# Performance work log

Measured on AMD Instinct MI355X. Metric: run time of the kernel, lower is better.

The kernel has to match this reference:

```python
import jax, jax.numpy as jnp
import numpy as np

N = 20000      # nodes
E = 200000     # edges (before self loops)
H = 8          # heads
C = 256        # out_channels per head
IN = 256       # in_channels
OUT = 250      # final linear out


def setup_inputs() -> dict:
    key = jax.random.key(0)
    ks = jax.random.split(key, 8)
    x = jax.random.normal(ks[0], (N, IN), jnp.float32)
    edge_index = jax.random.randint(ks[1], (2, E), 0, N)
    # GATConv params (lin has no bias in PyG; bias is on the conv output)
    W_gat = jax.random.normal(ks[2], (IN, H * C), jnp.float32) * 0.02
    att_src = jax.random.normal(ks[3], (H, C), jnp.float32) * 0.1
    att_dst = jax.random.normal(ks[4], (H, C), jnp.float32) * 0.1
    b_gat = jnp.zeros((H * C,), jnp.float32)
    # conv1: 1x1 conv with 1 in/out channel -> scalar weight + scalar bias
    conv_w = jax.random.normal(ks[5], (), jnp.float32)
    conv_b = jnp.zeros((), jnp.float32)
    W_lin = jax.random.normal(ks[6], (C, OUT), jnp.float32) * 0.02
    b_lin = jnp.zeros((OUT,), jnp.float32)
    return dict(x=x, edge_index=edge_index, W_gat=W_gat, att_src=att_src,
                att_dst=att_dst, b_gat=b_gat, conv_w=conv_w, conv_b=conv_b,
                W_lin=W_lin, b_lin=b_lin)


def reference(x, edge_index, W_gat, att_src, att_dst, b_gat, conv_w, conv_b, W_lin, b_lin):
    # --- GATConv (PyG defaults: add_self_loops=True, negative_slope=0.2, concat=True) ---
    loops = jnp.arange(N)
    src = jnp.concatenate([edge_index[0], loops])  # [E+N]
    dst = jnp.concatenate([edge_index[1], loops])
    xh = (x @ W_gat).reshape(N, H, C)              # [N,H,C]
    a_s = jnp.einsum('nhc,hc->nh', xh, att_src)    # [N,H]
    a_d = jnp.einsum('nhc,hc->nh', xh, att_dst)
    e = jax.nn.leaky_relu(a_s[src] + a_d[dst], 0.2)  # [E+N, H]
    # segment softmax over edges sharing a destination node
    m = jax.ops.segment_max(e, dst, num_segments=N)
    m = jnp.where(jnp.isfinite(m), m, 0.0)
    ex = jnp.exp(e - m[dst])
    s = jax.ops.segment_sum(ex, dst, num_segments=N)
    alpha = ex / (s[dst] + 1e-16)                  # [E+N, H]
    msg = xh[src] * alpha[:, :, None]              # [E+N, H, C]  (dominant traffic)
    agg = jax.ops.segment_sum(msg, dst, num_segments=N)  # [N,H,C]
    agg = agg + b_gat.reshape(H, C)
    # --- head split / pool / 1x1 conv / head softmax / fuse ---
    z = agg.transpose(1, 0, 2)                     # [H,N,C]  (torch z is [H,1,N,C])
    pooled = z.mean(axis=(1, 2))                   # [H] global avg pool
    g = jax.nn.relu(pooled * conv_w + conv_b)
    w = jax.nn.softmax(g, axis=0)                  # softmax over heads (dim=0)
    fuse = jnp.einsum('hnc,h->nc', z, w)           # sum over heads of z * w
    Hf = jax.nn.relu(fuse + x)                     # residual with input features
    return Hf @ W_lin + b_lin                      # [N, 250]
```

## Files before the change

### kernel.cpp

```cpp
#include <hip/hip_runtime.h>
#include <hip/hip_bf16.h>


typedef __attribute__((ext_vector_type(8))) short short8v;
typedef __attribute__((ext_vector_type(4))) float float4v;

__device__ __forceinline__ unsigned f2bfu(float f) {
  unsigned u = __float_as_uint(f);
  return (u + 0x7fffu + ((u >> 16) & 1u)) >> 16;
}
__device__ __forceinline__ float bfu_lo(unsigned u) { return __uint_as_float(u << 16); }
__device__ __forceinline__ float bfu_hi(unsigned u) { return __uint_as_float(u & 0xffff0000u); }
__device__ __forceinline__ unsigned pack2(float a, float b) { return f2bfu(a) | (f2bfu(b) << 16); }

__device__ __forceinline__ void ld8(const float* p, float* v) {
  float4 a = ((const float4*)p)[0], b = ((const float4*)p)[1];
  v[0] = a.x; v[1] = a.y; v[2] = a.z; v[3] = a.w;
  v[4] = b.x; v[5] = b.y; v[6] = b.z; v[7] = b.w;
}

__device__ __forceinline__ float bcast(float x, int e) {
  return __uint_as_float((unsigned)__builtin_amdgcn_readlane((int)__float_as_uint(x), e));
}

__device__ __forceinline__ void gll16(const void* g, void* l) {
  __builtin_amdgcn_global_load_lds(
      (__attribute__((address_space(1))) void*)const_cast<void*>(g),
      (__attribute__((address_space(3))) void*)(l), 16, 0, 0);
}

__global__ __launch_bounds__(256) void prep1_kernel(
    const float* __restrict__ W_lin, short* __restrict__ wlT,
    const float* __restrict__ W, const float* __restrict__ att_s,
    const float* __restrict__ att_d, float* __restrict__ ws_s,
    float* __restrict__ ws_d, float* __restrict__ ws_r,
    const int* __restrict__ ei, int* __restrict__ deg) {
  __shared__ float smem[4096];
  int b = blockIdx.x;
  int t = threadIdx.x;
  if (b < 64) {
    float (*tile)[33] = (float(*)[33])smem;
    int tx = t & 31, ty = t >> 5;
    int c0 = (b & 7) * 32, r0 = (b >> 3) * 32;
    #pragma unroll
    for (int j = ty; j < 32; j += 8) {
      int r = r0 + j, c = c0 + tx;
      tile[j][tx] = (c < 250) ? W_lin[(size_t)r * 250 + c] : 0.f;
    }
    __syncthreads();
    #pragma unroll
    for (int j = ty; j < 32; j += 8) {
      int c = c0 + j, r = r0 + tx;
      wlT[(size_t)c * 256 + r] = (short)f2bfu(tile[tx][j]);
    }
  } else if (b < 96) {
    float* sas = smem;
    float* sad = smem + 2048;
    for (int i = t; i < 2048; i += 256) { sas[i] = att_s[i]; sad[i] = att_d[i]; }
    __syncthreads();
    int kk = t >> 5, h = (t >> 2) & 7, q = t & 3;
    int k = (b - 64) * 8 + kk;
    const float4* wr = (const float4*)(W + (size_t)k * 2048 + h * 256 + q * 64);
    const float* as = sas + h * 256 + q * 64;
    const float* ad = sad + h * 256 + q * 64;
    float s = 0.f, dd = 0.f, r = 0.f;
    #pragma unroll
    for (int c4 = 0; c4 < 16; ++c4) {
      float4 wv = wr[c4];
      int c = c4 * 4;
      s  += wv.x * as[c] + wv.y * as[c + 1] + wv.z * as[c + 2] + wv.w * as[c + 3];
      dd += wv.x * ad[c] + wv.y * ad[c + 1] + wv.z * ad[c + 2] + wv.w * ad[c + 3];
      r  += wv.x + wv.y + wv.z + wv.w;
    }
    #pragma unroll
    for (int off = 1; off < 4; off <<= 1) {
      s += __shfl_xor(s, off);
      dd += __shfl_xor(dd, off);
      r += __shfl_xor(r, off);
    }
    if (q == 0) {
      int g = k * 8 + h;
      ws_s[g] = s;
      ws_d[g] = dd;
      ws_r[g] = r;
    }
  } else {
    int e = (b - 96) * 256 + t;
    if (e < 200000) atomicAdd(&deg[ei[200000 + e]], 1);
  }
}

__global__ __launch_bounds__(256) void asd_kernel(const float* __restrict__ x,
    const float* __restrict__ ws_s, const float* __restrict__ ws_d,
    float* __restrict__ a_s, float* __restrict__ a_d, short* __restrict__ x_bf) {
  __shared__ float ls[2048], ld2[2048];
  int tid = threadIdx.x;
  for (int i = tid; i < 2048; i += 256) { ls[i] = ws_s[i]; ld2[i] = ws_d[i]; }
  __syncthreads();
  int node = blockIdx.x * 32 + (tid >> 3);
  int h = tid & 7;
  const float4* xr = (const float4*)(x + (size_t)node * 256);
  float as = 0.f, ad = 0.f;
  #pragma unroll 1
  for (int g = 0; g < 8; ++g) {
    bool own = (g == h);
    int bufi[16];
    #pragma unroll
    for (int j = 0; j < 8; ++j) {
      int k4 = g * 8 + j;
      float4 v = xr[k4];
      int k8 = k4 * 32 + h;
      as += v.x * ls[k8] + v.y * ls[k8 + 8] + v.z * ls[k8 + 16] + v.w * ls[k8 + 24];
      ad += v.x * ld2[k8] + v.y * ld2[k8 + 8] + v.z * ld2[k8 + 16] + v.w * ld2[k8 + 24];
      bufi[2 * j] = (int)pack2(v.x, v.y);
      bufi[2 * j + 1] = (int)pack2(v.z, v.w);
    }
    if (own) {
      int4* dst = (int4*)(x_bf + (size_t)node * 256 + h * 32);
      dst[0] = make_int4(bufi[0], bufi[1], bufi[2], bufi[3]);
      dst[1] = make_int4(bufi[4], bufi[5], bufi[6], bufi[7]);
      dst[2] = make_int4(bufi[8], bufi[9], bufi[10], bufi[11]);
      dst[3] = make_int4(bufi[12], bufi[13], bufi[14], bufi[15]);
    }
  }
  a_s[node * 8 + h] = as;
  a_d[node * 8 + h] = ad;
}

template <int EPI>
__global__ __launch_bounds__(256, 4) void gemm_kernel(
    const short* __restrict__ A, const short* __restrict__ BT,
    int M, int K,
    short* __restrict__ Cb, float* __restrict__ Cf,
    const float* __restrict__ bias, const float* __restrict__ xres, int Nout) {
  int g = blockIdx.x;
  int xk = g & 7, tt = g >> 3;
  int it = xk + 8 * (tt >> 2);
  if (it >= ((M + 63) >> 6)) return;
  int m0 = it << 6;
  int n0 = (tt & 3) << 6;

  __shared__ short lA[64 * 64];
  __shared__ short lB[64 * 64];
  int tid = threadIdx.x;
  int wave = tid >> 6, lane = tid & 63;
  int wm = wave >> 1, wn = wave & 1;
  int lr = lane & 15, lq = lane >> 4;

  float4v acc[2][2];
  #pragma unroll
  for (int i = 0; i < 2; ++i)
    #pragma unroll
    for (int j = 0; j < 2; ++j) acc[i][j] = (float4v){0.f, 0.f, 0.f, 0.f};

  int lc = (lane & 7) ^ (lane >> 3);
  const short* pA[2];
  const short* pB[2];
  #pragma unroll
  for (int p = 0; p < 2; ++p) {
    int rl = wave * 16 + p * 8 + (lane >> 3);
    int ar = m0 + rl;
    if (ar >= M) ar = M - 1;
    pA[p] = A + (size_t)ar * K + lc * 8;
    pB[p] = BT + (size_t)(n0 + rl) * K + lc * 8;
  }

  for (int k0 = 0; k0 < K; k0 += 64) {
    __syncthreads();
    #pragma unroll
    for (int p = 0; p < 2; ++p) {
      gll16(pA[p] + k0, lA + (wave * 16 + p * 8) * 64);
      gll16(pB[p] + k0, lB + (wave * 16 + p * 8) * 64);
    }
    __syncthreads();
    #pragma unroll
    for (int ks = 0; ks < 2; ++ks) {
      int phys = (((ks * 4 + lq) ^ (lr & 7))) * 8;
      short8v af[2], bfv[2];
      #pragma unroll
      for (int i = 0; i < 2; ++i)
        af[i] = *(const short8v*)(lA + (wm * 32 + i * 16 + lr) * 64 + phys);
      #pragma unroll
      for (int j = 0; j < 2; ++j)
        bfv[j] = *(const short8v*)(lB + (wn * 32 + j * 16 + lr) * 64 + phys);
      #pragma unroll
      for (int i = 0; i < 2; ++i)
        #pragma unroll
        for (int j = 0; j < 2; ++j)
          acc[i][j] = __builtin_amdgcn_mfma_f32_16x16x32_bf16(af[i], bfv[j], acc[i][j], 0, 0, 0);
    }
  }

  #pragma unroll
  for (int i = 0; i < 2; ++i) {
    #pragma unroll
    for (int jj = 0; jj < 4; ++jj) {
      int row = m0 + wm * 32 + i * 16 + lq * 4 + jj;
      if (row >= M) continue;
      #pragma unroll
      for (int j = 0; j < 2; ++j) {
        int col = n0 + wn * 32 + j * 16 + lr;
        float v = acc[i][j][jj];
        if (EPI == 1) {
          if (col < Nout) Cf[(size_t)row * Nout + col] = v + bias[col];
        } else {
          float o = v + bias[col] + xres[(size_t)row * 256 + col];
          Cb[(size_t)row * 256 + col] = (short)f2bfu(fmaxf(o, 0.f));
        }
      }
    }
  }
}


__global__ __launch_bounds__(1024) void scan_kernel(const int* __restrict__ deg,
                                                    int* __restrict__ rowptr,
                                                    int* __restrict__ cursor, int n) {
  __shared__ int part[1024];
  int t = threadIdx.x;
  int base = t * 20;
  int loc[20];
  int run = 0;
  #pragma unroll
  for (int j = 0; j < 20; ++j) {
    int idx = base + j;
    int v = (idx < n) ? deg[idx] : 0;
    loc[j] = run;
    run += v;
  }
  part[t] = run;
  __syncthreads();
  for (int off = 1; off < 1024; off <<= 1) {
    int add = (t >= off) ? part[t - off] : 0;
    __syncthreads();
    part[t] += add;
    __syncthreads();
  }
  int off0 = (t > 0) ? part[t - 1] : 0;
  #pragma unroll
  for (int j = 0; j < 20; ++j) {
    int idx = base + j;
    if (idx < n) {
      int v = off0 + loc[j];
      rowptr[idx] = v;
      cursor[idx] = v;
    }
  }
  if (t == 1023) rowptr[n] = part[1023];
}

__global__ void scatter_kernel(const int* __restrict__ ei, int* __restrict__ cursor,
                               int* __restrict__ csr_src, int E) {
  int e = blockIdx.x * 256 + threadIdx.x;
  if (e < E) {
    int pos = atomicAdd(&cursor[ei[E + e]], 1);
    csr_src[pos] = ei[e];
  }
}

__global__ __launch_bounds__(64) void alphaz_kernel(
    const short* __restrict__ x_bf, const float* __restrict__ a_s,
    const float* __restrict__ a_d, const float* __restrict__ ws_r,
    const int* __restrict__ rowptr, const int* __restrict__ csr,
    short* __restrict__ u, float* __restrict__ pp) {
  int d = blockIdx.x;
  int lane = threadIdx.x;
  int cl = lane * 4;
  int beg = rowptr[d];
  int deg = rowptr[d + 1] - beg;
  int nb = deg + 1;

  float ad8[8];
  ld8(a_d + (size_t)d * 8, ad8);

  float acc[8][4];
  #pragma unroll
  for (int h = 0; h < 8; ++h)
    #pragma unroll
    for (int c = 0; c < 4; ++c) acc[h][c] = 0.f;
  float s8[8] = {0, 0, 0, 0, 0, 0, 0, 0};

  for (int base = 0; base < nb; base += 64) {
    int i = base + lane;
    bool act = i < nb;
    int srcv = d;
    if (i < deg) srcv = csr[beg + i];
    float ex[8];
    {
      float t8[8];
      ld8(a_s + (size_t)srcv * 8, t8);
      #pragma unroll
      for (int h = 0; h < 8; ++h) {
        float e = t8[h] + ad8[h];
        e = (e > 0.f) ? e : 0.2f * e;
        float xx = act ? __expf(e) : 0.f;
        ex[h] = xx;
        s8[h] += xx;
      }
    }
    int cnt = nb - base;
    if (cnt > 64) cnt = 64;
    for (int e = 0; e < cnt; ++e) {
      int sb = __builtin_amdgcn_readlane(srcv, e);
      uint2 v = *(const uint2*)(x_bf + (size_t)sb * 256 + cl);
      float q[8];
      #pragma unroll
      for (int h = 0; h < 8; ++h) q[h] = bcast(ex[h], e);
      float xv0 = bfu_lo(v.x), xv1 = bfu_hi(v.x);
      float xv2 = bfu_lo(v.y), xv3 = bfu_hi(v.y);
      #pragma unroll
      for (int h = 0; h < 8; ++h) {
        acc[h][0] += q[h] * xv0;
        acc[h][1] += q[h] * xv1;
        acc[h][2] += q[h] * xv2;
        acc[h][3] += q[h] * xv3;
      }
    }
  }

  #pragma unroll
  for (int off = 1; off < 64; off <<= 1)
    #pragma unroll
    for (int h = 0; h < 8; ++h) s8[h] += __shfl_xor(s8[h], off);
  float inv[8];
  #pragma unroll
  for (int h = 0; h < 8; ++h) inv[h] = 1.f / (s8[h] + 1e-16f);

  #pragma unroll
  for (int h = 0; h < 8; ++h) {
    uint2 ov;
    ov.x = pack2(acc[h][0] * inv[h], acc[h][1] * inv[h]);
    ov.y = pack2(acc[h][2] * inv[h], acc[h][3] * inv[h]);
    *(uint2*)(u + (size_t)d * 2048 + h * 256 + cl) = ov;
  }

  float ppl[8] = {0, 0, 0, 0, 0, 0, 0, 0};
  {
    const float4* wr = (const float4*)(ws_r + (size_t)cl * 8);
    #pragma unroll
    for (int c = 0; c < 4; ++c) {
      float4 wa = wr[c * 2], wb = wr[c * 2 + 1];
      float zc[8];
      #pragma unroll
      for (int h = 0; h < 8; ++h) zc[h] = acc[h][c] * inv[h];
      ppl[0] += zc[0] * wa.x; ppl[1] += zc[1] * wa.y;
      ppl[2] += zc[2] * wa.z; ppl[3] += zc[3] * wa.w;
      ppl[4] += zc[4] * wb.x; ppl[5] += zc[5] * wb.y;
      ppl[6] += zc[6] * wb.z; ppl[7] += zc[7] * wb.w;
    }
  }
  #pragma unroll
  for (int off = 1; off < 64; off <<= 1)
    #pragma unroll
    for (int h = 0; h < 8; ++h) ppl[h] += __shfl_xor(ppl[h], off);
  if (lane == 0) {
    ((float4*)(pp + (size_t)d * 8))[0] = make_float4(ppl[0], ppl[1], ppl[2], ppl[3]);
    ((float4*)(pp + (size_t)d * 8))[1] = make_float4(ppl[4], ppl[5], ppl[6], ppl[7]);
  }
}

__global__ __launch_bounds__(256) void reduce_pp_kernel(const float* __restrict__ pp,
                                                        float* __restrict__ pooled) {
  int tid = threadIdx.x;
  float loc[8] = {0, 0, 0, 0, 0, 0, 0, 0};
  for (int r = blockIdx.x * 256 + tid; r < 20000; r += 80 * 256) {
    float t[8];
    ld8(pp + (size_t)r * 8, t);
    #pragma unroll
    for (int h = 0; h < 8; ++h) loc[h] += t[h];
  }
  #pragma unroll
  for (int off = 1; off < 64; off <<= 1)
    #pragma unroll
    for (int h = 0; h < 8; ++h) loc[h] += __shfl_xor(loc[h], off);
  __shared__ float sred[4][8];
  int wave = tid >> 6, lane = tid & 63;
  if (lane == 0) {
    #pragma unroll
    for (int h = 0; h < 8; ++h) sred[wave][h] = loc[h];
  }
  __syncthreads();
  if (tid < 8) {
    atomicAdd(&pooled[tid], sred[0][tid] + sred[1][tid] + sred[2][tid] + sred[3][tid]);
  }
}

__global__ __launch_bounds__(256) void headwfb_kernel(const float* __restrict__ pooled,
    const float* __restrict__ b_gat, const float* __restrict__ conv_w,
    const float* __restrict__ conv_b, float* __restrict__ wsoft,
    float* __restrict__ fb) {
  __shared__ float sb[8];
  __shared__ float sw[8];
  int t = threadIdx.x;
  float v = 0.f;
  #pragma unroll
  for (int j = 0; j < 8; ++j) v += b_gat[t * 8 + j];
  #pragma unroll
  for (int off = 1; off < 32; off <<= 1) v += __shfl_xor(v, off);
  if ((t & 31) == 0) sb[t >> 5] = v;
  __syncthreads();
  if (t == 0) {
    const float invNC = 1.0f / (20000.0f * 256.0f);
    float g[8];
    float mx = -1e30f;
    #pragma unroll
    for (int h = 0; h < 8; ++h) {
      float pm = (pooled[h] + 20000.0f * sb[h]) * invNC;
      float gv = pm * conv_w[0] + conv_b[0];
      gv = fmaxf(gv, 0.f);
      g[h] = gv;
      mx = fmaxf(mx, gv);
    }
    float ssum = 0.f;
    #pragma unroll
    for (int h = 0; h < 8; ++h) { g[h] = __expf(g[h] - mx); ssum += g[h]; }
    #pragma unroll
    for (int h = 0; h < 8; ++h) {
      float w = g[h] / ssum;
      wsoft[h] = w;
      sw[h] = w;
    }
  }
  __syncthreads();
  float a = 0.f;
  #pragma unroll
  for (int h = 0; h < 8; ++h) a += sw[h] * b_gat[h * 256 + t];
  fb[t] = a;
}

__global__ void wmix_kernel(const float* __restrict__ W, const float* __restrict__ wsoft,
                            short* __restrict__ out) {
  __shared__ float tile[32][33];
  int tx = threadIdx.x, ty = threadIdx.y;
  int h = blockIdx.z;
  float wh = wsoft[h];
  int c0 = blockIdx.x * 32, k0 = blockIdx.y * 32;
  #pragma unroll
  for (int j = ty; j < 32; j += 8)
    tile[j][tx] = W[(size_t)(k0 + j) * 2048 + h * 256 + c0 + tx];
  __syncthreads();
  #pragma unroll
  for (int j = ty; j < 32; j += 8)
    out[(size_t)(c0 + j) * 2048 + h * 256 + k0 + tx] = (short)f2bfu(wh * tile[tx][j]);
}

extern "C" void kernel_launch(void* const* d_in, const int* in_sizes, int n_in,
                              void* d_out, int out_size, void* d_ws, size_t ws_size,
                              hipStream_t stream) {
  (void)in_sizes; (void)n_in; (void)out_size; (void)ws_size;
  const float* x      = (const float*)d_in[0];
  const int*   ei     = (const int*)d_in[1];
  const float* W_gat  = (const float*)d_in[2];
  const float* att_s  = (const float*)d_in[3];
  const float* att_d  = (const float*)d_in[4];
  const float* b_gat  = (const float*)d_in[5];
  const float* conv_w = (const float*)d_in[6];
  const float* conv_b = (const float*)d_in[7];
  const float* W_lin  = (const float*)d_in[8];
  const float* b_lin  = (const float*)d_in[9];
  float* out = (float*)d_out;

  char* p = (char*)d_ws;
  size_t off = 0;
  auto alloc = [&](size_t bytes) -> void* {
    void* r = p + off;
    off = (off + bytes + 255) & ~(size_t)255;
    return r;
  };
  short* x_bf   = (short*)alloc((size_t)20000 * 256 * 2);
  short* wmixT  = (short*)alloc((size_t)256 * 2048 * 2);
  short* wlT    = (short*)alloc((size_t)256 * 256 * 2);
  float* ws_s   = (float*)alloc(2048 * 4);
  float* ws_d   = (float*)alloc(2048 * 4);
  float* ws_r   = (float*)alloc(2048 * 4);
  float* a_s    = (float*)alloc((size_t)20000 * 8 * 4);
  float* a_d    = (float*)alloc((size_t)20000 * 8 * 4);
  int*   deg    = (int*)alloc(20000 * 4);
  float* pooled = (float*)alloc(8 * 4);
  float* wsoft  = (float*)alloc(8 * 4);
  float* fb     = (float*)alloc(256 * 4);
  int*   rowptr = (int*)alloc(20001 * 4);
  int*   cursor = (int*)alloc(20000 * 4);
  int*   csr    = (int*)alloc(200000 * 4);
  float* pp     = (float*)alloc((size_t)20000 * 8 * 4);
  short* u      = (short*)alloc((size_t)20000 * 2048 * 2);
  short* Hf     = x_bf;

  hipMemsetAsync(deg, 0, 20000 * 4, stream);
  hipMemsetAsync(pooled, 0, 8 * 4, stream);

  prep1_kernel<<<878, 256, 0, stream>>>(W_lin, wlT, W_gat, att_s, att_d,
                                        ws_s, ws_d, ws_r, ei, deg);
  scan_kernel<<<1, 1024, 0, stream>>>(deg, rowptr, cursor, 20000);
  asd_kernel<<<625, 256, 0, stream>>>(x, ws_s, ws_d, a_s, a_d, x_bf);
  scatter_kernel<<<782, 256, 0, stream>>>(ei, cursor, csr, 200000);
  alphaz_kernel<<<20000, 64, 0, stream>>>(x_bf, a_s, a_d, ws_r, rowptr, csr, u, pp);
  reduce_pp_kernel<<<80, 256, 0, stream>>>(pp, pooled);
  headwfb_kernel<<<1, 256, 0, stream>>>(pooled, b_gat, conv_w, conv_b, wsoft, fb);
  wmix_kernel<<<dim3(8, 8, 8), dim3(32, 8), 0, stream>>>(W_gat, wsoft, wmixT);
  gemm_kernel<2><<<1280, 256, 0, stream>>>(u, wmixT, 20000, 2048,
                                           Hf, nullptr, fb, x, 256);
  gemm_kernel<1><<<1280, 256, 0, stream>>>(Hf, wlT, 20000, 256,
                                           nullptr, out, b_lin, nullptr, 250);
}
```

Before: 175.2 us.

## Double-buffer GEMM LDS tiles and batch gather loads in aggregation loop

```diff
diff --git a/kernel.cpp b/kernel.cpp
--- a/kernel.cpp
+++ b/kernel.cpp
@@ -140,8 +140,8 @@
   int m0 = it << 6;
   int n0 = (tt & 3) << 6;
 
-  __shared__ short lA[64 * 64];
-  __shared__ short lB[64 * 64];
+  __shared__ short lA[2][64 * 64];
+  __shared__ short lB[2][64 * 64];
   int tid = threadIdx.x;
   int wave = tid >> 6, lane = tid & 63;
   int wm = wave >> 1, wn = wave & 1;
@@ -165,30 +165,41 @@
     pB[p] = BT + (size_t)(n0 + rl) * K + lc * 8;
   }
 
-  for (int k0 = 0; k0 < K; k0 += 64) {
-    __syncthreads();
+  auto stage = [&](int buf, int k0) {
     #pragma unroll
     for (int p = 0; p < 2; ++p) {
-      gll16(pA[p] + k0, lA + (wave * 16 + p * 8) * 64);
-      gll16(pB[p] + k0, lB + (wave * 16 + p * 8) * 64);
-    }
-    __syncthreads();
+      gll16(pA[p] + k0, &lA[buf][(wave * 16 + p * 8) * 64]);
+      gll16(pB[p] + k0, &lB[buf][(wave * 16 + p * 8) * 64]);
+    }
+  };
+
+  int nk = K >> 6;
+  stage(0, 0);
+  asm volatile("s_waitcnt vmcnt(0)" ::: "memory");
+  __builtin_amdgcn_s_barrier();
+
+  int cur = 0;
+  for (int t = 0; t < nk; ++t) {
+    if (t + 1 < nk) stage(cur ^ 1, (t + 1) << 6);
     #pragma unroll
     for (int ks = 0; ks < 2; ++ks) {
       int phys = (((ks * 4 + lq) ^ (lr & 7))) * 8;
       short8v af[2], bfv[2];
       #pragma unroll
       for (int i = 0; i < 2; ++i)
-        af[i] = *(const short8v*)(lA + (wm * 32 + i * 16 + lr) * 64 + phys);
+        af[i] = *(const short8v*)(&lA[cur][(wm * 32 + i * 16 + lr) * 64 + phys]);
       #pragma unroll
       for (int j = 0; j < 2; ++j)
-        bfv[j] = *(const short8v*)(lB + (wn * 32 + j * 16 + lr) * 64 + phys);
+        bfv[j] = *(const short8v*)(&lB[cur][(wn * 32 + j * 16 + lr) * 64 + phys]);
       #pragma unroll
       for (int i = 0; i < 2; ++i)
         #pragma unroll
         for (int j = 0; j < 2; ++j)
           acc[i][j] = __builtin_amdgcn_mfma_f32_16x16x32_bf16(af[i], bfv[j], acc[i][j], 0, 0, 0);
     }
+    asm volatile("s_waitcnt vmcnt(0)" ::: "memory");
+    __builtin_amdgcn_s_barrier();
+    cur ^= 1;
   }
 
   #pragma unroll
@@ -300,20 +311,30 @@
     }
     int cnt = nb - base;
     if (cnt > 64) cnt = 64;
-    for (int e = 0; e < cnt; ++e) {
-      int sb = __builtin_amdgcn_readlane(srcv, e);
-      uint2 v = *(const uint2*)(x_bf + (size_t)sb * 256 + cl);
-      float q[8];
-      #pragma unroll
-      for (int h = 0; h < 8; ++h) q[h] = bcast(ex[h], e);
-      float xv0 = bfu_lo(v.x), xv1 = bfu_hi(v.x);
-      float xv2 = bfu_lo(v.y), xv3 = bfu_hi(v.y);
-      #pragma unroll
-      for (int h = 0; h < 8; ++h) {
-        acc[h][0] += q[h] * xv0;
-        acc[h][1] += q[h] * xv1;
-        acc[h][2] += q[h] * xv2;
-        acc[h][3] += q[h] * xv3;
+    for (int e0 = 0; e0 < cnt; e0 += 8) {
+      uint2 vbuf[8];
+      #pragma unroll
+      for (int j = 0; j < 8; ++j) {
+        int e = e0 + j;
+        int sb = __builtin_amdgcn_readlane(srcv, (e < cnt) ? e : 0);
+        vbuf[j] = *(const uint2*)(x_bf + (size_t)sb * 256 + cl);
+      }
+      #pragma unroll
+      for (int j = 0; j < 8; ++j) {
+        int e = e0 + j;
+        bool a2 = e < cnt;
+        float q[8];
+        #pragma unroll
+        for (int h = 0; h < 8; ++h) q[h] = a2 ? bcast(ex[h], e) : 0.f;
+        float xv0 = bfu_lo(vbuf[j].x), xv1 = bfu_hi(vbuf[j].x);
+        float xv2 = bfu_lo(vbuf[j].y), xv3 = bfu_hi(vbuf[j].y);
+        #pragma unroll
+        for (int h = 0; h < 8; ++h) {
+          acc[h][0] += q[h] * xv0;
+          acc[h][1] += q[h] * xv1;
+          acc[h][2] += q[h] * xv2;
+          acc[h][3] += q[h] * xv3;
+        }
       }
     }
   }
```

Measured after the change: 196.8 us. 12.3% more time.
